# Kernel optimization log

Hardware: AMD Instinct MI355X
Metric: run time of the kernel (lower is better)

## Reference

```python
import jax, jax.numpy as jnp
from jax import lax
import numpy as np

K = 3        # kernel_size
PAD = 1      # zero padding applied to x before sampling
STRIDE = 1   # stride of the offset-predicting conv
B, C_IN, C_OUT, H, W = 8, 64, 64, 64, 64
N = K * K


def setup_inputs() -> dict:
    key = jax.random.key(0)
    k1, k2, k3 = jax.random.split(key, 3)
    x = jax.random.normal(k1, (B, C_IN, H, W), jnp.float32)
    W_off = jax.random.normal(k2, (2 * N, C_IN, 3, 3), jnp.float32) * 0.05
    b_off = jnp.zeros((2 * N,), jnp.float32)
    W_conv = jax.random.normal(k3, (C_OUT, C_IN, K, K), jnp.float32) * 0.05
    return {"x": x, "W_off": W_off, "b_off": b_off, "W_conv": W_conv}


def _deform_conv(x, W_off, b_off, W_conv):
    # offset conv: Conv2d(C_IN, 2*N, 3, padding=1, stride=STRIDE) with bias
    offset = lax.conv_general_dilated(
        x, W_off, (STRIDE, STRIDE), ((1, 1), (1, 1)),
        dimension_numbers=("NCHW", "OIHW", "NCHW")) + b_off[None, :, None, None]
    b, _, h, w = offset.shape

    # zero-pad input (nn.ZeroPad2d(PAD))
    xp = jnp.pad(x, ((0, 0), (0, 0), (PAD, PAD), (PAD, PAD)))
    Hp, Wp = xp.shape[2], xp.shape[3]

    # p_0: output-pixel base coords (1-based, stride-spaced), shape (h, w)
    p0x = jnp.arange(1, h * STRIDE + 1, STRIDE, dtype=x.dtype)[:, None] * jnp.ones((1, w), x.dtype)
    p0y = jnp.ones((h, 1), x.dtype) * jnp.arange(1, w * STRIDE + 1, STRIDE, dtype=x.dtype)[None, :]
    # p_n: kernel-relative offsets, flattened in 'ij' meshgrid order, shape (N,)
    kk = jnp.arange(-(K - 1) // 2, (K - 1) // 2 + 1, dtype=x.dtype)
    pnx = jnp.repeat(kk, K)
    pny = jnp.tile(kk, K)

    off = offset.transpose(0, 2, 3, 1)  # (b, h, w, 2N)
    px = p0x[None, :, :, None] + pnx[None, None, None, :] + off[..., :N]  # (b,h,w,N)
    py = p0y[None, :, :, None] + pny[None, None, None, :] + off[..., N:]

    # integer corners from detached p (p.detach().floor() in torch)
    pxd = lax.stop_gradient(px)
    pyd = lax.stop_gradient(py)
    qlt_x = jnp.clip(jnp.floor(pxd), 0, Hp - 1).astype(jnp.int32)
    qlt_y = jnp.clip(jnp.floor(pyd), 0, Wp - 1).astype(jnp.int32)
    qrb_x = jnp.clip(jnp.floor(pxd) + 1, 0, Hp - 1).astype(jnp.int32)
    qrb_y = jnp.clip(jnp.floor(pyd) + 1, 0, Wp - 1).astype(jnp.int32)

    # clamp p (differentiable)
    pxc = jnp.clip(px, 0, Hp - 1)
    pyc = jnp.clip(py, 0, Wp - 1)

    flt_x = qlt_x.astype(x.dtype); flt_y = qlt_y.astype(x.dtype)
    frb_x = qrb_x.astype(x.dtype); frb_y = qrb_y.astype(x.dtype)
    g_lt = (1 + (flt_x - pxc)) * (1 + (flt_y - pyc))
    g_rb = (1 - (frb_x - pxc)) * (1 - (frb_y - pyc))
    g_lb = (1 + (flt_x - pxc)) * (1 - (frb_y - pyc))  # q_lb = (qlt_x, qrb_y)
    g_rt = (1 - (frb_x - pxc)) * (1 + (flt_y - pyc))  # q_rt = (qrb_x, qlt_y)

    # gather: per-batch fancy indexing, (c,Hp,Wp)[:,qx,qy] -> (c,h,w,N)
    gather = jax.vmap(lambda xb, qx, qy: xb[:, qx, qy])
    x_lt = gather(xp, qlt_x, qlt_y)
    x_rb = gather(xp, qrb_x, qrb_y)
    x_lb = gather(xp, qlt_x, qrb_y)
    x_rt = gather(xp, qrb_x, qlt_y)

    xo = (g_lt[:, None] * x_lt + g_rb[:, None] * x_rb
          + g_lb[:, None] * x_lb + g_rt[:, None] * x_rt)  # (b,c,h,w,N)

    # reshape_x_offset: (b,c,h,w,kh*kw) -> (b,c,h*kh,w*kw)
    c = xo.shape[1]
    xo = xo.reshape(b, c, h, w, K, K).transpose(0, 1, 2, 4, 3, 5).reshape(b, c, h * K, w * K)

    # final conv: kernel K, stride K, no bias
    return lax.conv_general_dilated(
        xo, W_conv, (K, K), ((0, 0), (0, 0)),
        dimension_numbers=("NCHW", "OIHW", "NCHW"))


def reference(x, W_off, b_off, W_conv):
    return _deform_conv(x, W_off, b_off, W_conv)
```

## Files before the change

kernel.cpp:

```cpp
#include <hip/hip_runtime.h>
#include <hip/hip_bf16.h>


typedef unsigned int u32;
typedef unsigned short u16;
typedef short s8v __attribute__((ext_vector_type(8)));
typedef short s4v __attribute__((ext_vector_type(4)));
typedef float f4v __attribute__((ext_vector_type(4)));

#define XOS_STRIDE 592

__device__ __forceinline__ u16 f2bf(float f) {
  u32 u = __builtin_bit_cast(u32, f);
  u32 r = (u + 0x7FFFu + ((u >> 16) & 1u)) >> 16;
  return (u16)r;
}

__global__ __launch_bounds__(512, 4) void k01(
    const float* __restrict__ x,
    const float* __restrict__ wconv,
    const float* __restrict__ woff,
    const float* __restrict__ boff,
    u16* __restrict__ wfrag,
    float* __restrict__ offs_g,
    float* __restrict__ xT) {
  __shared__ float part[4608];
  __shared__ float tile[64][65];

  int bid = blockIdx.x;
  int b = bid & 7, h = bid >> 3;
  int bh = b * 64 + h;
  int t = threadIdx.x;
  int w = t & 63;
  int wv = __builtin_amdgcn_readfirstlane(t >> 6);
  const float* xb = x + b * 262144;

  int tid = bid * 512 + t;
  if (tid < 4608) {
    int nt = tid / 1152, ks = (tid / 64) % 18, lane = tid & 63;
    int co = nt * 16 + (lane & 15);
    int n = ks >> 1, s = ks & 1;
    int cl8 = (lane >> 4) << 3;
    u16* dst = wfrag + tid * 8;
    #pragma unroll
    for (int j = 0; j < 8; ++j) {
      int c = s * 32 + cl8 + j;
      dst[j] = f2bf(wconv[co * 576 + c * 9 + n]);
    }
  }

  bool lf = w > 0, rt = w < 63;
  float acc[18];
  #pragma unroll
  for (int o = 0; o < 18; ++o) acc[o] = 0.f;

  for (int cl = 0; cl < 8; ++cl) {
    int c = wv * 8 + cl;
    const float* xc = xb + c * 4096;
    float v[9];
    #pragma unroll
    for (int kh = 0; kh < 3; ++kh) {
      int hh = h + kh - 1;
      bool vr = (hh >= 0 && hh < 64);
      const float* row = xc + hh * 64;
      v[kh * 3 + 0] = (vr && lf) ? row[w - 1] : 0.f;
      v[kh * 3 + 1] = vr         ? row[w]     : 0.f;
      v[kh * 3 + 2] = (vr && rt) ? row[w + 1] : 0.f;
    }
    tile[c][w] = v[4];
    #pragma unroll
    for (int o = 0; o < 18; ++o) {
      const float* wo = woff + (o * 64 + c) * 9;
      acc[o] += v[0]*wo[0] + v[1]*wo[1] + v[2]*wo[2] + v[3]*wo[3]
              + v[4]*wo[4] + v[5]*wo[5] + v[6]*wo[6] + v[7]*wo[7]
              + v[8]*wo[8];
    }
  }

  if (wv >= 4) {
    float* reg = part + (wv - 4) * 1152;
    #pragma unroll
    for (int o = 0; o < 18; ++o)
      reg[o * 64 + w] = acc[o];
  }
  __syncthreads();
  if (wv < 4) {
    float* reg = part + wv * 1152;
    #pragma unroll
    for (int o = 0; o < 18; ++o)
      reg[o * 64 + w] += acc[o];
  }
  __syncthreads();
  float* og = offs_g + bh * 1152;
  for (int i = t; i < 1152; i += 512) {
    int o = i >> 6;
    og[i] = boff[o] + part[i] + part[1152 + i] + part[2304 + i] + part[3456 + i];
  }

  float* dstT = xT + bh * 4096;
  int c2 = t & 63, wr = t >> 6;
  #pragma unroll
  for (int i = 0; i < 8; ++i) {
    int w2 = wr * 8 + i;
    dstT[w2 * 64 + c2] = tile[c2][w2];
  }
}

__global__ __launch_bounds__(256, 4) void k2_sample(
    const float* __restrict__ xT,
    const float* __restrict__ offs_g,
    const u16*  __restrict__ wfrag,
    float* __restrict__ out) {
  __shared__ __align__(16) u16 xos[16 * XOS_STRIDE];

  int bid = blockIdx.x;
  int b = bid & 7;
  int r = bid >> 3;
  int h = r >> 2, wq = r & 3;
  int bh = b * 64 + h;
  int t = threadIdx.x;

  int cg4 = t & 15;
  int wls = t >> 4;
  int w_g = wq * 16 + wls;
  u32 qa[9];
  f4v gg[9];
  {
    const float* og = offs_g + bh * 1152 + w_g;
    #pragma unroll
    for (int n = 0; n < 9; ++n) {
      float ox = og[n * 64];
      float oy = og[(9 + n) * 64];
      float px = (float)(h + (n / 3)) + ox;
      float py = (float)(w_g + (n % 3)) + oy;
      float fx = floorf(px), fy = floorf(py);
      float pxc  = fminf(fmaxf(px, 0.f), 65.f);
      float pyc  = fminf(fmaxf(py, 0.f), 65.f);
      float fltx = fminf(fmaxf(fx, 0.f), 65.f);
      float flty = fminf(fmaxf(fy, 0.f), 65.f);
      float frbx = fminf(fmaxf(fx + 1.f, 0.f), 65.f);
      float frby = fminf(fmaxf(fy + 1.f, 0.f), 65.f);
      float ax = 1.f + fltx - pxc, bx = 1.f - frbx + pxc;
      float ay = 1.f + flty - pyc, by = 1.f - frby + pyc;
      float glt = ax * ay, grb = bx * by, glb = ax * by, grt = bx * ay;

      int ilt = (int)fltx, jlt = (int)flty, irb = (int)frbx, jrb = (int)frby;
      bool bi0 = (ilt >= 1 && ilt <= 64), bj0 = (jlt >= 1 && jlt <= 64);
      bool bi1 = (irb >= 1 && irb <= 64), bj1 = (jrb >= 1 && jrb <= 64);
      u32 i0 = bi0 ? (u32)(ilt - 1) : 0u;
      u32 j0 = bj0 ? (u32)(jlt - 1) : 0u;
      u32 i1 = bi1 ? (u32)(irb - 1) : 0u;
      u32 j1 = bj1 ? (u32)(jrb - 1) : 0u;
      qa[n] = i0 | (j0 << 8) | (i1 << 16) | (j1 << 24);
      f4v gv;
      gv[0] = (bi0 && bj0) ? glt : 0.f;
      gv[1] = (bi1 && bj1) ? grb : 0.f;
      gv[2] = (bi0 && bj1) ? glb : 0.f;
      gv[3] = (bi1 && bj0) ? grt : 0.f;
      gg[n] = gv;
    }
  }

  {
    const float* xq = xT + b * 262144 + cg4 * 4;
    u16* xrow = xos + wls * XOS_STRIDE + cg4 * 4;
    #pragma unroll
    for (int n = 0; n < 9; ++n) {
      u32 q = qa[n];
      f4v g = gg[n];
      int i0 = (int)(q & 255u) << 12;
      int j0 = (int)((q >> 8) & 255u) << 6;
      int i1 = (int)((q >> 16) & 255u) << 12;
      int j1 = (int)(q >> 24) << 6;
      f4v lt = *(const f4v*)(xq + i0 + j0);
      f4v rb = *(const f4v*)(xq + i1 + j1);
      f4v lb = *(const f4v*)(xq + i0 + j1);
      f4v rt = *(const f4v*)(xq + i1 + j0);
      f4v v  = g[0] * lt + g[1] * rb + g[2] * lb + g[3] * rt;
      s4v pk;
      pk[0] = (short)f2bf(v[0]);
      pk[1] = (short)f2bf(v[1]);
      pk[2] = (short)f2bf(v[2]);
      pk[3] = (short)f2bf(v[3]);
      *(s4v*)(xrow + n * 64) = pk;
    }
  }
  __syncthreads();

  {
    int wv = t >> 6;
    int lane = t & 63;
    int aoff = (lane & 15) * XOS_STRIDE + ((lane >> 4) << 3);
    const s8v* Wf = (const s8v*)wfrag;
    f4v acc = {0.f, 0.f, 0.f, 0.f};
    #pragma unroll
    for (int ks = 0; ks < 18; ++ks) {
      s8v a  = *(const s8v*)(xos + aoff + ks * 32);
      s8v b0 = Wf[(wv * 18 + ks) * 64 + lane];
      acc = __builtin_amdgcn_mfma_f32_16x16x32_bf16(a, b0, acc, 0, 0, 0);
    }
    int quad = lane >> 4;
    int co = wv * 16 + (lane & 15);
    *(f4v*)(out + b * 262144 + co * 4096 + h * 64 + wq * 16 + quad * 4) = acc;
  }
}

extern "C" void kernel_launch(void* const* d_in, const int* in_sizes, int n_in,
                              void* d_out, int out_size, void* d_ws, size_t ws_size,
                              hipStream_t stream) {
  const float *x = nullptr, *woff = nullptr, *boff = nullptr, *wconv = nullptr;
  for (int i = 0; i < n_in; ++i) {
    switch (in_sizes[i]) {
      case 2097152: x     = (const float*)d_in[i]; break;
      case 10368:   woff  = (const float*)d_in[i]; break;
      case 18:      boff  = (const float*)d_in[i]; break;
      case 36864:   wconv = (const float*)d_in[i]; break;
      default: break;
    }
  }
  if (!x)     x     = (const float*)d_in[0];
  if (!woff)  woff  = (const float*)d_in[1];
  if (!boff)  boff  = (const float*)d_in[2];
  if (!wconv) wconv = (const float*)d_in[3];
  float* out = (float*)d_out;

  u16*   wfrag  = (u16*)d_ws;
  float* xT     = (float*)((char*)d_ws + 131072);
  float* offs_g = (float*)((char*)d_ws + 8519680);

  k01<<<512, 512, 0, stream>>>(x, wconv, woff, boff, wfrag, offs_g, xT);
  k2_sample<<<2048, 256, 0, stream>>>(xT, offs_g, wfrag, out);
}
```

Measured before the change: 110.4 us.

## Move offset conv into sampling kernel as bf16 MFMA im2col GEMM

The scalar FP32 offset convolution in the first kernel is replaced by an im2col tile built in LDS inside the sampling kernel, followed by bf16 MFMA against pre-packed offset weights. The first kernel now only packs weights and transposes x, and the global offset buffer round-trip is gone. In exchange, offsets are computed in bf16, which can shift floor() decisions for sampling coordinates. The MFMA runs on a single wave per block while the other waves wait, and each block adds an extra LDS pass and barriers.

Result: faster. 94.95 us (-14.0%).

```diff
diff --git a/kernel.cpp b/kernel.cpp
--- a/kernel.cpp
+++ b/kernel.cpp
@@ -16,26 +16,18 @@
   return (u16)r;
 }
 
-__global__ __launch_bounds__(512, 4) void k01(
+__global__ __launch_bounds__(256) void k01(
     const float* __restrict__ x,
     const float* __restrict__ wconv,
     const float* __restrict__ woff,
-    const float* __restrict__ boff,
     u16* __restrict__ wfrag,
-    float* __restrict__ offs_g,
+    u16* __restrict__ wofrag,
     float* __restrict__ xT) {
-  __shared__ float part[4608];
   __shared__ float tile[64][65];
-
   int bid = blockIdx.x;
-  int b = bid & 7, h = bid >> 3;
-  int bh = b * 64 + h;
   int t = threadIdx.x;
-  int w = t & 63;
-  int wv = __builtin_amdgcn_readfirstlane(t >> 6);
-  const float* xb = x + b * 262144;
-
-  int tid = bid * 512 + t;
+  int tid = bid * 256 + t;
+
   if (tid < 4608) {
     int nt = tid / 1152, ks = (tid / 64) % 18, lane = tid & 63;
     int co = nt * 16 + (lane & 15);
@@ -48,89 +40,110 @@
       dst[j] = f2bf(wconv[co * 576 + c * 9 + n]);
     }
   }
-
-  bool lf = w > 0, rt = w < 63;
-  float acc[18];
+  if (tid >= 8192 && tid < 10496) {
+    int idx = tid - 8192;
+    int nt2 = idx / 1152, ks = (idx / 64) % 18, lane = idx & 63;
+    int o = nt2 * 16 + (lane & 15);
+    int n = ks >> 1, s = ks & 1;
+    int cl8 = (lane >> 4) << 3;
+    u16* dst = wofrag + idx * 8;
+    #pragma unroll
+    for (int j = 0; j < 8; ++j) {
+      int c = s * 32 + cl8 + j;
+      float v = (o < 18) ? woff[(o * 64 + c) * 9 + n] : 0.f;
+      dst[j] = f2bf(v);
+    }
+  }
+
+  int bh = ((bid & 7) << 6) | (bid >> 3);
+  const float* xb = x + (bh >> 6) * 262144 + (bh & 63) * 64;
+  int w = t & 63, cr = t >> 6;
   #pragma unroll
-  for (int o = 0; o < 18; ++o) acc[o] = 0.f;
-
-  for (int cl = 0; cl < 8; ++cl) {
-    int c = wv * 8 + cl;
-    const float* xc = xb + c * 4096;
-    float v[9];
-    #pragma unroll
-    for (int kh = 0; kh < 3; ++kh) {
-      int hh = h + kh - 1;
-      bool vr = (hh >= 0 && hh < 64);
-      const float* row = xc + hh * 64;
-      v[kh * 3 + 0] = (vr && lf) ? row[w - 1] : 0.f;
-      v[kh * 3 + 1] = vr         ? row[w]     : 0.f;
-      v[kh * 3 + 2] = (vr && rt) ? row[w + 1] : 0.f;
-    }
-    tile[c][w] = v[4];
-    #pragma unroll
-    for (int o = 0; o < 18; ++o) {
-      const float* wo = woff + (o * 64 + c) * 9;
-      acc[o] += v[0]*wo[0] + v[1]*wo[1] + v[2]*wo[2] + v[3]*wo[3]
-              + v[4]*wo[4] + v[5]*wo[5] + v[6]*wo[6] + v[7]*wo[7]
-              + v[8]*wo[8];
-    }
-  }
-
-  if (wv >= 4) {
-    float* reg = part + (wv - 4) * 1152;
-    #pragma unroll
-    for (int o = 0; o < 18; ++o)
-      reg[o * 64 + w] = acc[o];
-  }
-  __syncthreads();
-  if (wv < 4) {
-    float* reg = part + wv * 1152;
-    #pragma unroll
-    for (int o = 0; o < 18; ++o)
-      reg[o * 64 + w] += acc[o];
-  }
-  __syncthreads();
-  float* og = offs_g + bh * 1152;
-  for (int i = t; i < 1152; i += 512) {
-    int o = i >> 6;
-    og[i] = boff[o] + part[i] + part[1152 + i] + part[2304 + i] + part[3456 + i];
-  }
-
+  for (int i = 0; i < 16; ++i) {
+    int c = cr * 16 + i;
+    tile[c][w] = xb[c * 4096 + w];
+  }
+  __syncthreads();
   float* dstT = xT + bh * 4096;
   int c2 = t & 63, wr = t >> 6;
   #pragma unroll
-  for (int i = 0; i < 8; ++i) {
-    int w2 = wr * 8 + i;
+  for (int i = 0; i < 16; ++i) {
+    int w2 = wr * 16 + i;
     dstT[w2 * 64 + c2] = tile[c2][w2];
   }
 }
 
 __global__ __launch_bounds__(256, 4) void k2_sample(
     const float* __restrict__ xT,
-    const float* __restrict__ offs_g,
     const u16*  __restrict__ wfrag,
+    const u16*  __restrict__ wofrag,
+    const float* __restrict__ boff,
     float* __restrict__ out) {
-  __shared__ __align__(16) u16 xos[16 * XOS_STRIDE];
+  __shared__ __align__(16) u16 xim[16 * XOS_STRIDE];
+  __shared__ float offs_lds[288];
 
   int bid = blockIdx.x;
   int b = bid & 7;
   int r = bid >> 3;
   int h = r >> 2, wq = r & 3;
-  int bh = b * 64 + h;
   int t = threadIdx.x;
-
   int cg4 = t & 15;
   int wls = t >> 4;
   int w_g = wq * 16 + wls;
+  const float* xTb = xT + b * 262144;
+
+  {
+    const float* xq = xTb + cg4 * 4;
+    u16* xrow = xim + wls * XOS_STRIDE + cg4 * 4;
+    #pragma unroll
+    for (int n = 0; n < 9; ++n) {
+      int hh = h + (n / 3) - 1;
+      int ww = w_g + (n % 3) - 1;
+      f4v v = {0.f, 0.f, 0.f, 0.f};
+      if (hh >= 0 && hh < 64 && ww >= 0 && ww < 64)
+        v = *(const f4v*)(xq + (hh * 64 + ww) * 64);
+      s4v pk;
+      pk[0] = (short)f2bf(v[0]);
+      pk[1] = (short)f2bf(v[1]);
+      pk[2] = (short)f2bf(v[2]);
+      pk[3] = (short)f2bf(v[3]);
+      *(s4v*)(xrow + n * 64) = pk;
+    }
+  }
+  __syncthreads();
+
+  if (t < 64) {
+    int lane = t;
+    int aoff = (lane & 15) * XOS_STRIDE + ((lane >> 4) << 3);
+    const s8v* Wo = (const s8v*)wofrag;
+    f4v a0 = {0.f, 0.f, 0.f, 0.f}, a1 = {0.f, 0.f, 0.f, 0.f};
+    #pragma unroll
+    for (int ks = 0; ks < 18; ++ks) {
+      s8v a  = *(const s8v*)(xim + aoff + ks * 32);
+      a0 = __builtin_amdgcn_mfma_f32_16x16x32_bf16(a, Wo[ks * 64 + lane], a0, 0, 0, 0);
+      a1 = __builtin_amdgcn_mfma_f32_16x16x32_bf16(a, Wo[(18 + ks) * 64 + lane], a1, 0, 0, 0);
+    }
+    int quad = lane >> 4, ol = lane & 15;
+    float bo0 = boff[ol];
+    #pragma unroll
+    for (int r4 = 0; r4 < 4; ++r4)
+      offs_lds[ol * 16 + quad * 4 + r4] = a0[r4] + bo0;
+    if (ol < 2) {
+      float bo1 = boff[16 + ol];
+      #pragma unroll
+      for (int r4 = 0; r4 < 4; ++r4)
+        offs_lds[(16 + ol) * 16 + quad * 4 + r4] = a1[r4] + bo1;
+    }
+  }
+  __syncthreads();
+
   u32 qa[9];
   f4v gg[9];
   {
-    const float* og = offs_g + bh * 1152 + w_g;
     #pragma unroll
     for (int n = 0; n < 9; ++n) {
-      float ox = og[n * 64];
-      float oy = og[(9 + n) * 64];
+      float ox = offs_lds[n * 16 + wls];
+      float oy = offs_lds[(9 + n) * 16 + wls];
       float px = (float)(h + (n / 3)) + ox;
       float py = (float)(w_g + (n % 3)) + oy;
       float fx = floorf(px), fy = floorf(py);
@@ -160,10 +173,9 @@
       gg[n] = gv;
     }
   }
-
-  {
-    const float* xq = xT + b * 262144 + cg4 * 4;
-    u16* xrow = xos + wls * XOS_STRIDE + cg4 * 4;
+  {
+    const float* xq = xTb + cg4 * 4;
+    u16* xrow = xim + wls * XOS_STRIDE + cg4 * 4;
     #pragma unroll
     for (int n = 0; n < 9; ++n) {
       u32 q = qa[n];
@@ -195,7 +207,7 @@
     f4v acc = {0.f, 0.f, 0.f, 0.f};
     #pragma unroll
     for (int ks = 0; ks < 18; ++ks) {
-      s8v a  = *(const s8v*)(xos + aoff + ks * 32);
+      s8v a  = *(const s8v*)(xim + aoff + ks * 32);
       s8v b0 = Wf[(wv * 18 + ks) * 64 + lane];
       acc = __builtin_amdgcn_mfma_f32_16x16x32_bf16(a, b0, acc, 0, 0, 0);
     }
@@ -225,9 +237,9 @@
   float* out = (float*)d_out;
 
   u16*   wfrag  = (u16*)d_ws;
+  u16*   wofrag = (u16*)((char*)d_ws + 73728);
   float* xT     = (float*)((char*)d_ws + 131072);
-  float* offs_g = (float*)((char*)d_ws + 8519680);
-
-  k01<<<512, 512, 0, stream>>>(x, wconv, woff, boff, wfrag, offs_g, xT);
-  k2_sample<<<2048, 256, 0, stream>>>(xT, offs_g, wfrag, out);
-}
+
+  k01<<<512, 256, 0, stream>>>(x, wconv, woff, wfrag, wofrag, xT);
+  k2_sample<<<2048, 256, 0, stream>>>(xT, wfrag, wofrag, boff, out);
+}
```
